# Kernel tuning notes

Measured on AMD Instinct MI355X. Metric: run time of the kernel, lower is better.

## Reference

```python
import jax, jax.numpy as jnp
import numpy as np

L, B, E = 2048, 4, 1024
H = 8
D1 = 2048          # expand_ratio * E, multiple of H
HD = D1 // H       # head dim 256
MAX_L = 2048
EPS = 1e-8


def setup_inputs() -> dict:
    key = jax.random.key(0)
    ks = jax.random.split(key, 9)
    std = 0.02
    return {
        "x": jax.random.normal(ks[0], (L, B, E), jnp.float32),
        "Wu": jax.random.normal(ks[1], (D1, E), jnp.float32) * std,
        "bu": jax.random.normal(ks[2], (D1,), jnp.float32) * std,
        "Wv": jax.random.normal(ks[3], (D1, E), jnp.float32) * std,
        "bv": jax.random.normal(ks[4], (D1,), jnp.float32) * std,
        "Wo": jax.random.normal(ks[5], (E, D1), jnp.float32) * std,
        "bo": jax.random.normal(ks[6], (E,), jnp.float32) * std,
        "zero": jax.random.normal(ks[7], (H, 1), jnp.float32) * 0.1,   # Toeplitz coef, offset 0
        "pos": jax.random.normal(ks[8], (H, MAX_L - 1), jnp.float32) * 0.1,  # offsets 1..n-1
    }


def _simple_rmsnorm(x):
    d = x.shape[-1]
    rms = jnp.linalg.norm(x, axis=-1, keepdims=True) * (d ** -0.5)
    return x / (rms + EPS)


def _toeplitz_causal_fft(v, zero, pos):
    # v: (b, h, n, hd); causal Toeplitz mixing along n via FFT long conv
    n = v.shape[-2]
    coef = jnp.concatenate([zero, pos[:, : n - 1]], axis=-1)  # (h, n)
    m = 2 * n
    cf = jnp.fft.rfft(coef, m, axis=-1)                  # (h, m//2+1)
    vf = jnp.fft.rfft(v, m, axis=-2)                     # (b, h, m//2+1, hd)
    out = jnp.fft.irfft(cf[None, :, :, None] * vf, m, axis=-2)
    return out[:, :, :n, :]


def reference(x, Wu, bu, Wv, bv, Wo, bo, zero, pos):
    # x: (n, b, e) fairseq layout
    n, b, e = x.shape
    shortcut = x
    xn = _simple_rmsnorm(x)                               # pre_norm (SimpleRMSNorm, no params)
    u = jax.nn.silu(jnp.einsum('nbe,de->nbd', xn, Wu) + bu)   # (n,b,d1)
    v = jax.nn.silu(jnp.einsum('nbe,de->nbd', xn, Wv) + bv)   # (n,b,d1)
    # 'n b (h d) -> b h n d'
    vh = v.transpose(1, 0, 2).reshape(b, n, H, HD).transpose(0, 2, 1, 3)
    oh = _toeplitz_causal_fft(vh, zero, pos)              # (b,h,n,hd)
    o = oh.transpose(0, 2, 1, 3).reshape(b, n, D1).transpose(1, 0, 2)  # (n,b,d1)
    o = u * o                                             # gating
    out = jnp.einsum('nbd,ed->nbe', o, Wo) + bo + shortcut
    return out
```

## Files before the change

kernel.cpp:

```cpp
#include <hip/hip_runtime.h>
#include <cstdint>
#include <cstddef>

#define LQ   2048
#define BQ   4
#define EQ   1024
#define HQ   8
#define D1Q  2048
#define HDQ  256
#define NBQ  (LQ*BQ)

typedef __bf16 bf16_t;
typedef __bf16 bf16x8 __attribute__((ext_vector_type(8)));
typedef __bf16 bf16x4 __attribute__((ext_vector_type(4)));
typedef float  f32x4  __attribute__((ext_vector_type(4)));

#define GAS1(p) ((const __attribute__((address_space(1))) void*)(p))
#define LAS3(p) ((__attribute__((address_space(3))) void*)(p))


__global__ __launch_bounds__(256) void convert_kernel(
    const float* __restrict__ Wu, const float* __restrict__ Wv,
    const float* __restrict__ Wo,
    bf16_t* __restrict__ Wub, bf16_t* __restrict__ Wvb,
    bf16_t* __restrict__ Wob)
{
    const size_t i = (size_t)blockIdx.x * 256 + threadIdx.x;
    if (i < (size_t)D1Q * EQ) {
        Wub[i] = (bf16_t)Wu[i];
        Wvb[i] = (bf16_t)Wv[i];
        Wob[i] = (bf16_t)Wo[i];
    }
}

__global__ __launch_bounds__(256) void build_toep_tiles(
    const float* __restrict__ zero, const float* __restrict__ pos,
    bf16_t* __restrict__ Atiles)
{
    const int q = blockIdx.x;
    const int h = blockIdx.y;
    const int doff = (q - 3) * 32;
    const int tid = threadIdx.x;
    bf16_t* dst = Atiles + ((size_t)h * 64 + q) * (128 * 32);
    const int e0 = tid * 16;
    const int r = e0 >> 5;
    const int cbase = e0 & 31;
    bf16_t vals[16];
    #pragma unroll
    for (int j = 0; j < 16; ++j) {
        const int d = doff + r - (cbase + j);
        float v = 0.f;
        if (d == 0) v = zero[h];
        else if (d > 0) v = pos[(size_t)h * (LQ - 1) + d - 1];
        vals[j] = (bf16_t)v;
    }
    *(bf16x8*)(dst + e0)     = *(bf16x8*)(vals);
    *(bf16x8*)(dst + e0 + 8) = *(bf16x8*)(vals + 8);
}

__global__ __launch_bounds__(256) void rmsnorm_kernel(
    const float* __restrict__ x, bf16_t* __restrict__ xn)
{
    const int row = blockIdx.x;
    const int tid = threadIdx.x;
    const float4 v = ((const float4*)(x + (size_t)row * EQ))[tid];
    float ss = v.x*v.x + v.y*v.y + v.z*v.z + v.w*v.w;
    #pragma unroll
    for (int m = 32; m >= 1; m >>= 1) ss += __shfl_xor(ss, m, 64);
    __shared__ float red[4];
    const int wid = tid >> 6, lane = tid & 63;
    if (lane == 0) red[wid] = ss;
    __syncthreads();
    const float tot = red[0] + red[1] + red[2] + red[3];
    const float inv = 1.f / (sqrtf(tot * (1.f / EQ)) + 1e-8f);
    bf16x4 o;
    o[0] = (bf16_t)(v.x * inv); o[1] = (bf16_t)(v.y * inv);
    o[2] = (bf16_t)(v.z * inv); o[3] = (bf16_t)(v.w * inv);
    *(bf16x4*)(xn + (size_t)row * EQ + tid * 4) = o;
}


template<int MI, int WM, int WN, int MODE>
__global__ __launch_bounds__(512, 2) void gemm8p(
    const bf16_t* __restrict__ A, const bf16_t* __restrict__ Bm,
    int K, int N,
    const float* __restrict__ bias, const float* __restrict__ res,
    bf16_t* __restrict__ Cb, float* __restrict__ Cf)
{
    constexpr int BM = WM * MI * 16;
    constexpr int BN = WN * 64;
    constexpr int ABYTES = BM * 128;
    constexpr int BBYTES = BN * 128;
    constexpr int BSTRIDE = ABYTES + BBYTES;
    constexpr int CA = BM / 64;
    constexpr int CB = BN / 64;
    constexpr int NPH = 2 * (MI / 4);
    static_assert(BM == 256, "staging assumes BM=256");
    static_assert(MODE != 1 || (MI == 8 && WN == 4), "MODE1 geometry");
    __shared__ alignas(16) char smem[2 * BSTRIDE];

    const int nwg   = gridDim.x * gridDim.y;
    const int bid   = blockIdx.y * gridDim.x + blockIdx.x;
    const int chunkw = nwg >> 3;
    const int sb    = (bid & 7) * chunkw + (bid >> 3);
    const int bx    = sb % gridDim.x;
    const int by    = sb / gridDim.x;

    const int tid  = threadIdx.x;
    const int wid  = tid >> 6;
    const int lane = tid & 63;
    const int frow = lane & 15;
    const int c    = lane >> 4;
    const int m0 = by * BM;
    const int n0 = bx * BN;
    const int wm = wid / WN, wn = wid % WN;
    const int wrm = wm * (MI * 16);
    const int wrn = wn * 64;

    const int g = frow & 7;
    const int offA0 = (wrm + frow) * 128 + ((c ^ g) << 4);
    const int offA1 = offA0 ^ 64;
    const int offB0 = (wrn + frow) * 128 + ((c ^ g) << 4);
    const int offB1 = offB0 ^ 64;

    const int rl = tid >> 3;
    const int ps = tid & 7;
    const int ls = ps ^ (rl & 7);
    const size_t lda2 = (size_t)K * 2;
    const char* sA = (const char*)A  + (size_t)(m0 + rl) * lda2 + ls * 16;
    const char* sB = (const char*)Bm + (size_t)(n0 + rl) * lda2 + ls * 16;

    auto STAGE_A = [&](int bf, int kt) {
        char* d = smem + bf * BSTRIDE + wid * 1024;
        #pragma unroll
        for (int cl = 0; cl < CA; ++cl)
            __builtin_amdgcn_global_load_lds(
                GAS1(sA + (size_t)cl * 64 * lda2 + (size_t)kt * 128),
                LAS3(d + cl * 8192), 16, 0, 0);
    };
    auto STAGE_B = [&](int bf, int kt) {
        char* d = smem + bf * BSTRIDE + ABYTES + wid * 1024;
        #pragma unroll
        for (int cl = 0; cl < CB; ++cl)
            __builtin_amdgcn_global_load_lds(
                GAS1(sB + (size_t)cl * 64 * lda2 + (size_t)kt * 128),
                LAS3(d + cl * 8192), 16, 0, 0);
    };

    f32x4 acc[MI][4];
    #pragma unroll
    for (int i = 0; i < MI; ++i)
        #pragma unroll
        for (int j = 0; j < 4; ++j) acc[i][j] = (f32x4){0.f, 0.f, 0.f, 0.f};

    const int NT = K >> 6;

    STAGE_A(0, 0); STAGE_B(0, 0);
    asm volatile("s_waitcnt vmcnt(0)" ::: "memory");
    __builtin_amdgcn_s_barrier();

    int buf = 0;
    for (int t = 0; t < NT; ++t) {
        const char* bA = smem + buf * BSTRIDE;
        const char* bB = bA + ABYTES;
        const bool pf = (t + 1 < NT);
        const int nb = buf ^ 1;
        bf16x8 av[4], bv[4];

        #pragma unroll
        for (int kk = 0; kk < 2; ++kk) {
            #pragma unroll
            for (int mh = 0; mh < MI / 4; ++mh) {
                constexpr int MH = MI / 4;
                const int p = kk * MH + mh;
                #pragma unroll
                for (int i = 0; i < 4; ++i)
                    av[i] = *(const bf16x8*)(bA + (mh * 4 + i) * 2048 + (kk ? offA1 : offA0));
                if (mh == 0) {
                    #pragma unroll
                    for (int i = 0; i < 4; ++i)
                        bv[i] = *(const bf16x8*)(bB + i * 2048 + (kk ? offB1 : offB0));
                }
                if (pf && p == 0) STAGE_A(nb, t + 1);
                if (pf && p == 1) STAGE_B(nb, t + 1);
                __builtin_amdgcn_s_barrier();
                __builtin_amdgcn_s_setprio(1);
                #pragma unroll
                for (int i = 0; i < 4; ++i)
                    #pragma unroll
                    for (int ni = 0; ni < 4; ++ni)
                        acc[mh * 4 + i][ni] = __builtin_amdgcn_mfma_f32_16x16x32_bf16(
                            av[i], bv[ni], acc[mh * 4 + i][ni], 0, 0, 0);
                __builtin_amdgcn_s_setprio(0);
                if (p == NPH - 1) {
                    if (pf) asm volatile("s_waitcnt vmcnt(0)" ::: "memory");
                }
                __builtin_amdgcn_s_barrier();
            }
        }
        buf ^= 1;
    }

    if constexpr (MODE == 1) {
        const int hh = n0 >> 8;
        float bb[4];
        #pragma unroll
        for (int ni = 0; ni < 4; ++ni) bb[ni] = bias[n0 + wrn + ni * 16 + frow];

        #pragma unroll
        for (int p = 0; p < 2; ++p) {
            __syncthreads();
            bf16_t* chunk = (bf16_t*)smem + wid * 4224;
            #pragma unroll
            for (int mi = 0; mi < 8; ++mi) {
                #pragma unroll
                for (int nio = 0; nio < 2; ++nio) {
                    const int ni = p * 2 + nio;
                    const int nl = nio * 16 + frow;
                    #pragma unroll
                    for (int j = 0; j < 4; ++j) {
                        float v = acc[mi][ni][j] + bb[ni];
                        v = v / (1.f + __expf(-v));
                        chunk[nl * 132 + j * 32 + mi * 4 + c] = (bf16_t)v;
                    }
                }
            }
            __syncthreads();
            const int nl  = lane & 31;
            const int bh2 = lane >> 5;
            const int hd  = wrn + p * 32 + nl;
            const int t0  = (m0 + wrm) >> 2;
            #pragma unroll
            for (int bi = 0; bi < 2; ++bi) {
                const int b2 = bh2 * 2 + bi;
                const bf16_t* src = chunk + nl * 132 + b2 * 32;
                bf16_t* dst = Cb + (((size_t)hh * 4 + b2) * 256 + hd) * (size_t)LQ + t0;
                #pragma unroll
                for (int q = 0; q < 4; ++q)
                    *(bf16x8*)(dst + q * 8) = *(const bf16x8*)(src + q * 8);
            }
        }
        return;
    }

    const int fq = c * 4;
    #pragma unroll
    for (int mi = 0; mi < MI; ++mi) {
        #pragma unroll
        for (int ni = 0; ni < 4; ++ni) {
            const int gn = n0 + wrn + ni * 16 + frow;
            #pragma unroll
            for (int j = 0; j < 4; ++j) {
                const int gm = m0 + wrm + mi * 16 + fq + j;
                float v = acc[mi][ni][j];
                if constexpr (MODE == 0) {
                    v += bias[gn];
                    v = v / (1.f + __expf(-v));
                    Cb[(size_t)gm * N + gn] = (bf16_t)v;
                } else {
                    v += bias[gn] + res[(size_t)gm * N + gn];
                    Cf[(size_t)gm * N + gn] = v;
                }
            }
        }
    }
}

__global__ __launch_bounds__(512, 4) void gemm_toep8p(
    const bf16_t* __restrict__ VT, const bf16_t* __restrict__ Atiles,
    const bf16_t* __restrict__ U, bf16_t* __restrict__ O)
{
    constexpr int BSTRIDE = 24576;
    __shared__ alignas(16) char smem[3 * BSTRIDE];

    const int bid   = blockIdx.x;
    const int m_blk = 15 - (bid >> 5);
    const int sub   = bid & 31;
    const int h     = sub >> 2;
    const int n0    = (sub & 3) * 256;
    const int m0    = m_blk * 128;

    const int tid  = threadIdx.x;
    const int wid  = tid >> 6;
    const int lane = tid & 63;
    const int frow = lane & 15;
    const int c    = lane >> 4;
    const int wrm  = (wid >> 2) * 64;
    const int wrn  = (wid & 3) * 64;

    const int Ra = wrm + frow;
    const int ga = (Ra ^ (Ra >> 2)) & 3;
    const int offA = Ra * 64 + ((c ^ ga) << 4);
    const int Rb = wrn + frow;
    const int gb = (Rb ^ (Rb >> 2)) & 3;
    const int offB = 8192 + Rb * 64 + ((c ^ gb) << 4);

    const int sr   = tid >> 2;
    const int slot = tid & 3;
    const int gs   = (sr ^ (sr >> 2)) & 3;
    const int soff = (slot ^ gs) << 4;

    const char* Ah = (const char*)(Atiles + (size_t)h * 64 * 4096);
    const size_t ldb = (size_t)LQ * 2;
    const char* srcB  = (const char*)VT + ((size_t)h * 1024 + n0 + sr) * ldb + soff;
    const char* srcB2 = srcB + 128 * ldb;

    auto STAGE_A = [&](int buf, int kt) {
        const int q = 4 * m_blk + 3 - kt;
        const char* s = Ah + (size_t)q * 8192 + (size_t)sr * 64 + soff;
        __builtin_amdgcn_global_load_lds(GAS1(s),
                                         LAS3(smem + buf * BSTRIDE + wid * 1024), 16, 0, 0);
    };
    auto STAGE_B = [&](int buf, int kt) {
        char* d = smem + buf * BSTRIDE + 8192 + wid * 1024;
        __builtin_amdgcn_global_load_lds(GAS1(srcB  + (size_t)kt * 64), LAS3(d), 16, 0, 0);
        __builtin_amdgcn_global_load_lds(GAS1(srcB2 + (size_t)kt * 64), LAS3(d + 8192), 16, 0, 0);
    };

    f32x4 acc[4][4];
    #pragma unroll
    for (int i = 0; i < 4; ++i)
        #pragma unroll
        for (int j = 0; j < 4; ++j) acc[i][j] = (f32x4){0.f, 0.f, 0.f, 0.f};

    const int NT = 4 * m_blk + 4;

    STAGE_A(0, 0); STAGE_B(0, 0);
    STAGE_A(1, 1); STAGE_B(1, 1);
    asm volatile("s_waitcnt vmcnt(3)" ::: "memory");
    __builtin_amdgcn_s_barrier();

    int buf = 0;
    for (int kq = 0; kq < NT; ++kq) {
        const char* base = smem + buf * BSTRIDE;
        int pbuf = buf + 2; if (pbuf >= 3) pbuf -= 3;
        const bool pf = (kq < NT - 2);

        bf16x8 av[4], bv[4];
        #pragma unroll
        for (int i = 0; i < 4; ++i)
            av[i] = *(const bf16x8*)(base + offA + i * 1024);
        #pragma unroll
        for (int i = 0; i < 2; ++i)
            bv[i] = *(const bf16x8*)(base + offB + i * 1024);
        if (pf) STAGE_A(pbuf, kq + 2);
        __builtin_amdgcn_s_barrier();
        __builtin_amdgcn_s_setprio(1);
        #pragma unroll
        for (int mi = 0; mi < 4; ++mi)
            #pragma unroll
            for (int ni = 0; ni < 2; ++ni)
                acc[mi][ni] = __builtin_amdgcn_mfma_f32_16x16x32_bf16(
                    av[mi], bv[ni], acc[mi][ni], 0, 0, 0);
        __builtin_amdgcn_s_setprio(0);
        __builtin_amdgcn_s_barrier();

        #pragma unroll
        for (int i = 2; i < 4; ++i)
            bv[i] = *(const bf16x8*)(base + offB + i * 1024);
        if (pf) STAGE_B(pbuf, kq + 2);
        __builtin_amdgcn_s_barrier();
        __builtin_amdgcn_s_setprio(1);
        #pragma unroll
        for (int mi = 0; mi < 4; ++mi)
            #pragma unroll
            for (int ni = 2; ni < 4; ++ni)
                acc[mi][ni] = __builtin_amdgcn_mfma_f32_16x16x32_bf16(
                    av[mi], bv[ni], acc[mi][ni], 0, 0, 0);
        __builtin_amdgcn_s_setprio(0);

        if (kq < NT - 1) {
            if (kq <= NT - 3) asm volatile("s_waitcnt vmcnt(3)" ::: "memory");
            else              asm volatile("s_waitcnt vmcnt(0)" ::: "memory");
            __builtin_amdgcn_s_barrier();
        }
        buf = (buf == 2) ? 0 : buf + 1;
    }

    const int fq = c * 4;
    #pragma unroll
    for (int mi = 0; mi < 4; ++mi) {
        #pragma unroll
        for (int ni = 0; ni < 4; ++ni) {
            const int nn = n0 + wrn + ni * 16 + frow;
            const int b  = nn >> 8, hd = nn & 255;
            #pragma unroll
            for (int j = 0; j < 4; ++j) {
                const int t = m0 + wrm + mi * 16 + fq + j;
                const size_t idx = ((size_t)t * BQ + b) * D1Q + h * HDQ + hd;
                const float uval = (float)U[idx];
                O[idx] = (bf16_t)(uval * acc[mi][ni][j]);
            }
        }
    }
}


extern "C" void kernel_launch(void* const* d_in, const int* in_sizes, int n_in,
                              void* d_out, int out_size, void* d_ws, size_t ws_size,
                              hipStream_t stream)
{
    const float* x    = (const float*)d_in[0];
    const float* Wu   = (const float*)d_in[1];
    const float* bu   = (const float*)d_in[2];
    const float* Wv   = (const float*)d_in[3];
    const float* bv   = (const float*)d_in[4];
    const float* Wo   = (const float*)d_in[5];
    const float* bo   = (const float*)d_in[6];
    const float* zero = (const float*)d_in[7];
    const float* pos  = (const float*)d_in[8];
    float* out = (float*)d_out;

    char* ws = (char*)d_ws;
    size_t off = 0;
    auto alloc = [&](size_t bytes) {
        char* p = ws + off;
        off += (bytes + 255) & ~(size_t)255;
        return p;
    };
    bf16_t* xn     = (bf16_t*)alloc((size_t)NBQ * EQ * 2);
    bf16_t* Wub    = (bf16_t*)alloc((size_t)D1Q * EQ * 2);
    bf16_t* Wvb    = (bf16_t*)alloc((size_t)D1Q * EQ * 2);
    bf16_t* Wob    = (bf16_t*)alloc((size_t)EQ * D1Q * 2);
    bf16_t* Atiles = (bf16_t*)alloc((size_t)HQ * 64 * 4096 * 2);
    bf16_t* Ub     = (bf16_t*)alloc((size_t)NBQ * D1Q * 2);
    bf16_t* VTb    = (bf16_t*)alloc((size_t)NBQ * D1Q * 2);
    bf16_t* Ob     = (bf16_t*)alloc((size_t)NBQ * D1Q * 2);

    convert_kernel<<<8192, 256, 0, stream>>>(Wu, Wv, Wo, Wub, Wvb, Wob);
    build_toep_tiles<<<dim3(64, 8), 256, 0, stream>>>(zero, pos, Atiles);
    rmsnorm_kernel<<<NBQ, 256, 0, stream>>>(x, xn);

    dim3 g1(D1Q / 256, NBQ / 256);
    gemm8p<8, 2, 4, 0><<<g1, 512, 0, stream>>>(xn, Wub, EQ, D1Q, bu, nullptr, Ub, nullptr);
    gemm8p<8, 2, 4, 1><<<g1, 512, 0, stream>>>(xn, Wvb, EQ, D1Q, bv, nullptr, VTb, nullptr);

    gemm_toep8p<<<512, 512, 0, stream>>>(VTb, Atiles, Ub, Ob);

    dim3 g2(EQ / 128, NBQ / 256);
    gemm8p<4, 4, 2, 2><<<g2, 512, 0, stream>>>(Ob, Wob, D1Q, EQ, bo, x, nullptr, out);
}
```

Baseline: 208.5 us.

## Switch GEMMs to BK=32 triple-buffered pipeline with one barrier per k-step

Rewrites the generic GEMM main loop from a double-buffered 64-wide K tile with several barriers per step into a triple-buffered 32-wide K tile. Loads run two steps ahead and each step needs only one barrier. The LDS swizzle is adapted to the 64-byte rows. The U projection now uses a smaller 256x128 tile, and launch-bounds occupancy becomes a template parameter. The Toeplitz GEMM drops its split-phase B loads and extra barriers, and its occupancy hint is lowered. The goal is less barrier and synchronisation overhead and deeper prefetch, at the cost of more loop iterations and different occupancy.

```diff
diff --git a/kernel.cpp b/kernel.cpp
--- a/kernel.cpp
+++ b/kernel.cpp
@@ -80,8 +80,8 @@
 }
 
 
-template<int MI, int WM, int WN, int MODE>
-__global__ __launch_bounds__(512, 2) void gemm8p(
+template<int MI, int WM, int WN, int MODE, int WPB>
+__global__ __launch_bounds__(512, WPB) void gemm_p(
     const bf16_t* __restrict__ A, const bf16_t* __restrict__ Bm,
     int K, int N,
     const float* __restrict__ bias, const float* __restrict__ res,
@@ -89,20 +89,18 @@
 {
     constexpr int BM = WM * MI * 16;
     constexpr int BN = WN * 64;
-    constexpr int ABYTES = BM * 128;
-    constexpr int BBYTES = BN * 128;
+    constexpr int ABYTES = BM * 64;
+    constexpr int BBYTES = BN * 64;
     constexpr int BSTRIDE = ABYTES + BBYTES;
-    constexpr int CA = BM / 64;
-    constexpr int CB = BN / 64;
-    constexpr int NPH = 2 * (MI / 4);
+    constexpr int CB = BN / 128;
     static_assert(BM == 256, "staging assumes BM=256");
     static_assert(MODE != 1 || (MI == 8 && WN == 4), "MODE1 geometry");
-    __shared__ alignas(16) char smem[2 * BSTRIDE];
+    __shared__ alignas(16) char smem[3 * BSTRIDE];
 
     const int nwg   = gridDim.x * gridDim.y;
-    const int bid   = blockIdx.y * gridDim.x + blockIdx.x;
+    const int bid0  = blockIdx.y * gridDim.x + blockIdx.x;
     const int chunkw = nwg >> 3;
-    const int sb    = (bid & 7) * chunkw + (bid >> 3);
+    const int sb    = (bid0 & 7) * chunkw + (bid0 >> 3);
     const int bx    = sb % gridDim.x;
     const int by    = sb / gridDim.x;
 
@@ -117,35 +115,27 @@
     const int wrm = wm * (MI * 16);
     const int wrn = wn * 64;
 
-    const int g = frow & 7;
-    const int offA0 = (wrm + frow) * 128 + ((c ^ g) << 4);
-    const int offA1 = offA0 ^ 64;
-    const int offB0 = (wrn + frow) * 128 + ((c ^ g) << 4);
-    const int offB1 = offB0 ^ 64;
-
-    const int rl = tid >> 3;
-    const int ps = tid & 7;
-    const int ls = ps ^ (rl & 7);
+    const int g = (frow >> 1) & 3;
+    const int offA0 = (wrm + frow) * 64 + ((c ^ g) << 4);
+    const int offB0 = ABYTES + (wrn + frow) * 64 + ((c ^ g) << 4);
+
+    const int rA   = tid >> 2;
+    const int soff = (((tid & 3) ^ ((rA >> 1) & 3)) << 4);
     const size_t lda2 = (size_t)K * 2;
-    const char* sA = (const char*)A  + (size_t)(m0 + rl) * lda2 + ls * 16;
-    const char* sB = (const char*)Bm + (size_t)(n0 + rl) * lda2 + ls * 16;
-
-    auto STAGE_A = [&](int bf, int kt) {
-        char* d = smem + bf * BSTRIDE + wid * 1024;
-        #pragma unroll
-        for (int cl = 0; cl < CA; ++cl)
-            __builtin_amdgcn_global_load_lds(
-                GAS1(sA + (size_t)cl * 64 * lda2 + (size_t)kt * 128),
-                LAS3(d + cl * 8192), 16, 0, 0);
+    const char* sA = (const char*)A  + (size_t)(m0 + rA) * lda2 + soff;
+    const char* sB = (const char*)Bm + (size_t)(n0 + rA) * lda2 + soff;
+
+    auto STAGE = [&](int bf, int kt) {
+        char* dA = smem + bf * BSTRIDE + wid * 1024;
+        __builtin_amdgcn_global_load_lds(GAS1(sA + (size_t)kt * 64), LAS3(dA), 16, 0, 0);
+        __builtin_amdgcn_global_load_lds(GAS1(sA + 128 * lda2 + (size_t)kt * 64),
+                                         LAS3(dA + 8192), 16, 0, 0);
+        char* dB = smem + bf * BSTRIDE + ABYTES + wid * 1024;
+        __builtin_amdgcn_global_load_lds(GAS1(sB + (size_t)kt * 64), LAS3(dB), 16, 0, 0);
+        if constexpr (CB == 2)
+            __builtin_amdgcn_global_load_lds(GAS1(sB + 128 * lda2 + (size_t)kt * 64),
+                                             LAS3(dB + 8192), 16, 0, 0);
     };
-    auto STAGE_B = [&](int bf, int kt) {
-        char* d = smem + bf * BSTRIDE + ABYTES + wid * 1024;
-        #pragma unroll
-        for (int cl = 0; cl < CB; ++cl)
-            __builtin_amdgcn_global_load_lds(
-                GAS1(sB + (size_t)cl * 64 * lda2 + (size_t)kt * 128),
-                LAS3(d + cl * 8192), 16, 0, 0);
-    };
 
     f32x4 acc[MI][4];
     #pragma unroll
@@ -153,52 +143,43 @@
         #pragma unroll
         for (int j = 0; j < 4; ++j) acc[i][j] = (f32x4){0.f, 0.f, 0.f, 0.f};
 
-    const int NT = K >> 6;
-
-    STAGE_A(0, 0); STAGE_B(0, 0);
-    asm volatile("s_waitcnt vmcnt(0)" ::: "memory");
+    const int NT = K >> 5;
+
+    STAGE(0, 0); STAGE(1, 1);
+    if constexpr (CB == 1) asm volatile("s_waitcnt vmcnt(3)" ::: "memory");
+    else                   asm volatile("s_waitcnt vmcnt(4)" ::: "memory");
     __builtin_amdgcn_s_barrier();
 
-    int buf = 0;
+    int cur = 0, pb = 2;
     for (int t = 0; t < NT; ++t) {
-        const char* bA = smem + buf * BSTRIDE;
-        const char* bB = bA + ABYTES;
-        const bool pf = (t + 1 < NT);
-        const int nb = buf ^ 1;
-        bf16x8 av[4], bv[4];
-
-        #pragma unroll
-        for (int kk = 0; kk < 2; ++kk) {
-            #pragma unroll
-            for (int mh = 0; mh < MI / 4; ++mh) {
-                constexpr int MH = MI / 4;
-                const int p = kk * MH + mh;
-                #pragma unroll
-                for (int i = 0; i < 4; ++i)
-                    av[i] = *(const bf16x8*)(bA + (mh * 4 + i) * 2048 + (kk ? offA1 : offA0));
-                if (mh == 0) {
-                    #pragma unroll
-                    for (int i = 0; i < 4; ++i)
-                        bv[i] = *(const bf16x8*)(bB + i * 2048 + (kk ? offB1 : offB0));
-                }
-                if (pf && p == 0) STAGE_A(nb, t + 1);
-                if (pf && p == 1) STAGE_B(nb, t + 1);
-                __builtin_amdgcn_s_barrier();
-                __builtin_amdgcn_s_setprio(1);
-                #pragma unroll
-                for (int i = 0; i < 4; ++i)
-                    #pragma unroll
-                    for (int ni = 0; ni < 4; ++ni)
-                        acc[mh * 4 + i][ni] = __builtin_amdgcn_mfma_f32_16x16x32_bf16(
-                            av[i], bv[ni], acc[mh * 4 + i][ni], 0, 0, 0);
-                __builtin_amdgcn_s_setprio(0);
-                if (p == NPH - 1) {
-                    if (pf) asm volatile("s_waitcnt vmcnt(0)" ::: "memory");
-                }
-                __builtin_amdgcn_s_barrier();
-            }
-        }
-        buf ^= 1;
+        const char* base = smem + cur * BSTRIDE;
+        bf16x8 av[MI], bv[4];
+        #pragma unroll
+        for (int i = 0; i < MI; ++i)
+            av[i] = *(const bf16x8*)(base + offA0 + i * 1024);
+        #pragma unroll
+        for (int i = 0; i < 4; ++i)
+            bv[i] = *(const bf16x8*)(base + offB0 + i * 1024);
+        if (t + 2 < NT) STAGE(pb, t + 2);
+        __builtin_amdgcn_s_setprio(1);
+        #pragma unroll
+        for (int mi = 0; mi < MI; ++mi)
+            #pragma unroll
+            for (int ni = 0; ni < 4; ++ni)
+                acc[mi][ni] = __builtin_amdgcn_mfma_f32_16x16x32_bf16(
+                    av[mi], bv[ni], acc[mi][ni], 0, 0, 0);
+        __builtin_amdgcn_s_setprio(0);
+        if (t + 1 < NT) {
+            if (t + 2 < NT) {
+                if constexpr (CB == 1) asm volatile("s_waitcnt vmcnt(3)" ::: "memory");
+                else                   asm volatile("s_waitcnt vmcnt(4)" ::: "memory");
+            } else {
+                asm volatile("s_waitcnt vmcnt(0)" ::: "memory");
+            }
+            __builtin_amdgcn_s_barrier();
+        }
+        cur = (cur == 2) ? 0 : cur + 1;
+        pb  = (pb  == 2) ? 0 : pb  + 1;
     }
 
     if constexpr (MODE == 1) {
@@ -266,11 +247,12 @@
     }
 }
 
-__global__ __launch_bounds__(512, 4) void gemm_toep8p(
+__global__ __launch_bounds__(512, 2) void gemm_toep_p(
     const bf16_t* __restrict__ VT, const bf16_t* __restrict__ Atiles,
     const bf16_t* __restrict__ U, bf16_t* __restrict__ O)
 {
-    constexpr int BSTRIDE = 24576;
+    constexpr int ABYTES = 8192;
+    constexpr int BSTRIDE = ABYTES + 16384;
     __shared__ alignas(16) char smem[3 * BSTRIDE];
 
     const int bid   = blockIdx.x;
@@ -288,34 +270,26 @@
     const int wrm  = (wid >> 2) * 64;
     const int wrn  = (wid & 3) * 64;
 
-    const int Ra = wrm + frow;
-    const int ga = (Ra ^ (Ra >> 2)) & 3;
-    const int offA = Ra * 64 + ((c ^ ga) << 4);
-    const int Rb = wrn + frow;
-    const int gb = (Rb ^ (Rb >> 2)) & 3;
-    const int offB = 8192 + Rb * 64 + ((c ^ gb) << 4);
-
-    const int sr   = tid >> 2;
-    const int slot = tid & 3;
-    const int gs   = (sr ^ (sr >> 2)) & 3;
-    const int soff = (slot ^ gs) << 4;
-
-    const char* Ah = (const char*)(Atiles + (size_t)h * 64 * 4096);
+    const int g = (frow >> 1) & 3;
+    const int offA0 = (wrm + frow) * 64 + ((c ^ g) << 4);
+    const int offB0 = ABYTES + (wrn + frow) * 64 + ((c ^ g) << 4);
+
+    const int rA   = tid >> 2;
+    const int soff = (((tid & 3) ^ ((rA >> 1) & 3)) << 4);
+    const char* Ah = (const char*)Atiles + (size_t)h * 64 * 8192;
     const size_t ldb = (size_t)LQ * 2;
-    const char* srcB  = (const char*)VT + ((size_t)h * 1024 + n0 + sr) * ldb + soff;
-    const char* srcB2 = srcB + 128 * ldb;
-
-    auto STAGE_A = [&](int buf, int kt) {
+    const char* sB = (const char*)VT + ((size_t)h * 1024 + n0 + rA) * ldb + soff;
+
+    auto STAGE = [&](int bf, int kt) {
         const int q = 4 * m_blk + 3 - kt;
-        const char* s = Ah + (size_t)q * 8192 + (size_t)sr * 64 + soff;
-        __builtin_amdgcn_global_load_lds(GAS1(s),
-                                         LAS3(smem + buf * BSTRIDE + wid * 1024), 16, 0, 0);
+        __builtin_amdgcn_global_load_lds(
+            GAS1(Ah + (size_t)q * 8192 + (size_t)rA * 64 + soff),
+            LAS3(smem + bf * BSTRIDE + wid * 1024), 16, 0, 0);
+        char* dB = smem + bf * BSTRIDE + ABYTES + wid * 1024;
+        __builtin_amdgcn_global_load_lds(GAS1(sB + (size_t)kt * 64), LAS3(dB), 16, 0, 0);
+        __builtin_amdgcn_global_load_lds(GAS1(sB + 128 * ldb + (size_t)kt * 64),
+                                         LAS3(dB + 8192), 16, 0, 0);
     };
-    auto STAGE_B = [&](int buf, int kt) {
-        char* d = smem + buf * BSTRIDE + 8192 + wid * 1024;
-        __builtin_amdgcn_global_load_lds(GAS1(srcB  + (size_t)kt * 64), LAS3(d), 16, 0, 0);
-        __builtin_amdgcn_global_load_lds(GAS1(srcB2 + (size_t)kt * 64), LAS3(d + 8192), 16, 0, 0);
-    };
 
     f32x4 acc[4][4];
     #pragma unroll
@@ -325,56 +299,36 @@
 
     const int NT = 4 * m_blk + 4;
 
-    STAGE_A(0, 0); STAGE_B(0, 0);
-    STAGE_A(1, 1); STAGE_B(1, 1);
+    STAGE(0, 0); STAGE(1, 1);
     asm volatile("s_waitcnt vmcnt(3)" ::: "memory");
     __builtin_amdgcn_s_barrier();
 
-    int buf = 0;
-    for (int kq = 0; kq < NT; ++kq) {
-        const char* base = smem + buf * BSTRIDE;
-        int pbuf = buf + 2; if (pbuf >= 3) pbuf -= 3;
-        const bool pf = (kq < NT - 2);
-
+    int cur = 0, pb = 2;
+    for (int t = 0; t < NT; ++t) {
+        const char* base = smem + cur * BSTRIDE;
         bf16x8 av[4], bv[4];
         #pragma unroll
         for (int i = 0; i < 4; ++i)
-            av[i] = *(const bf16x8*)(base + offA + i * 1024);
-        #pragma unroll
-        for (int i = 0; i < 2; ++i)
-            bv[i] = *(const bf16x8*)(base + offB + i * 1024);
-        if (pf) STAGE_A(pbuf, kq + 2);
-        __builtin_amdgcn_s_barrier();
+            av[i] = *(const bf16x8*)(base + offA0 + i * 1024);
+        #pragma unroll
+        for (int i = 0; i < 4; ++i)
+            bv[i] = *(const bf16x8*)(base + offB0 + i * 1024);
+        if (t + 2 < NT) STAGE(pb, t + 2);
         __builtin_amdgcn_s_setprio(1);
         #pragma unroll
         for (int mi = 0; mi < 4; ++mi)
             #pragma unroll
-            for (int ni = 0; ni < 2; ++ni)
+            for (int ni = 0; ni < 4; ++ni)
                 acc[mi][ni] = __builtin_amdgcn_mfma_f32_16x16x32_bf16(
                     av[mi], bv[ni], acc[mi][ni], 0, 0, 0);
         __builtin_amdgcn_s_setprio(0);
-        __builtin_amdgcn_s_barrier();
-
-        #pragma unroll
-        for (int i = 2; i < 4; ++i)
-            bv[i] = *(const bf16x8*)(base + offB + i * 1024);
-        if (pf) STAGE_B(pbuf, kq + 2);
-        __builtin_amdgcn_s_barrier();
-        __builtin_amdgcn_s_setprio(1);
-        #pragma unroll
-        for (int mi = 0; mi < 4; ++mi)
-            #pragma unroll
-            for (int ni = 2; ni < 4; ++ni)
-                acc[mi][ni] = __builtin_amdgcn_mfma_f32_16x16x32_bf16(
-                    av[mi], bv[ni], acc[mi][ni], 0, 0, 0);
-        __builtin_amdgcn_s_setprio(0);
-
-        if (kq < NT - 1) {
-            if (kq <= NT - 3) asm volatile("s_waitcnt vmcnt(3)" ::: "memory");
-            else              asm volatile("s_waitcnt vmcnt(0)" ::: "memory");
+        if (t + 1 < NT) {
+            if (t + 2 < NT) asm volatile("s_waitcnt vmcnt(3)" ::: "memory");
+            else            asm volatile("s_waitcnt vmcnt(0)" ::: "memory");
             __builtin_amdgcn_s_barrier();
         }
-        buf = (buf == 2) ? 0 : buf + 1;
+        cur = (cur == 2) ? 0 : cur + 1;
+        pb  = (pb  == 2) ? 0 : pb  + 1;
     }
 
     const int fq = c * 4;
@@ -431,12 +385,13 @@
     build_toep_tiles<<<dim3(64, 8), 256, 0, stream>>>(zero, pos, Atiles);
     rmsnorm_kernel<<<NBQ, 256, 0, stream>>>(x, xn);
 
-    dim3 g1(D1Q / 256, NBQ / 256);
-    gemm8p<8, 2, 4, 0><<<g1, 512, 0, stream>>>(xn, Wub, EQ, D1Q, bu, nullptr, Ub, nullptr);
-    gemm8p<8, 2, 4, 1><<<g1, 512, 0, stream>>>(xn, Wvb, EQ, D1Q, bv, nullptr, VTb, nullptr);
-
-    gemm_toep8p<<<512, 512, 0, stream>>>(VTb, Atiles, Ub, Ob);
+    dim3 gU(D1Q / 128, NBQ / 256);
+    gemm_p<4, 4, 2, 0, 2><<<gU, 512, 0, stream>>>(xn, Wub, EQ, D1Q, bu, nullptr, Ub, nullptr);
+    dim3 gV(D1Q / 256, NBQ / 256);
+    gemm_p<8, 2, 4, 1, 1><<<gV, 512, 0, stream>>>(xn, Wvb, EQ, D1Q, bv, nullptr, VTb, nullptr);
+
+    gemm_toep_p<<<512, 512, 0, stream>>>(VTb, Atiles, Ub, Ob);
 
     dim3 g2(EQ / 128, NBQ / 256);
-    gemm8p<4, 4, 2, 2><<<g2, 512, 0, stream>>>(Ob, Wob, D1Q, EQ, bo, x, nullptr, out);
-}
+    gemm_p<4, 4, 2, 2, 2><<<g2, 512, 0, stream>>>(Ob, Wob, D1Q, EQ, bo, x, nullptr, out);
+}
```

Result: no change. 206.8 us (-0.8%).
